# Performance work log

Measured on AMD Instinct MI355X. Metric: run time of the kernel, lower is better.

The kernel has to match this reference:

```python
import jax, jax.numpy as jnp
import numpy as np

INPUT_SIZE = 1024
NUM_QUBITS = 12
EMBED_SIZE = 2 ** NUM_QUBITS  # 4096
BATCH = 4096


def setup_inputs() -> dict:
    key = jax.random.key(0)
    k_x, k_w, k_p = jax.random.split(key, 3)
    x = jax.random.normal(k_x, (BATCH, INPUT_SIZE), dtype=jnp.float32)
    quantum_weights = jax.random.normal(k_w, (INPUT_SIZE, EMBED_SIZE), dtype=jnp.float32)
    quantum_phases = jax.random.normal(k_p, (INPUT_SIZE, NUM_QUBITS), dtype=jnp.float32)
    return {"x": x, "quantum_weights": quantum_weights, "quantum_phases": quantum_phases}


def reference(x, quantum_weights, quantum_phases):
    # Original: out[b] = Re( sum_j exp(i * mean(phases[j]) * x[b,j]) * W[j,:] ).
    # W is real, so the real part is sum_j cos(mean(phases[j]) * x[b,j]) * W[j,:],
    # i.e. a cosine-modulated matmul.
    phase_mean = jnp.mean(quantum_phases, axis=1)          # [input_size]
    coef = jnp.cos(x * phase_mean[None, :])                # [batch, input_size]
    return coef @ quantum_weights                          # [batch, embed_size]
```

## Files before the change

### kernel.cpp

```cpp
#include <hip/hip_runtime.h>
#include <hip/hip_bf16.h>


#define K_DIM 1024
#define N_DIM 4096
#define B_DIM 4096
#define NQ 12

typedef __attribute__((ext_vector_type(8))) _Float16 f16x8;
typedef __attribute__((ext_vector_type(4))) float f32x4;


__global__ void pm_kernel(const float* __restrict__ phases, float* __restrict__ pm) {
    int j = blockIdx.x * 256 + threadIdx.x;
    if (j < K_DIM) {
        float s = 0.f;
#pragma unroll
        for (int q = 0; q < NQ; ++q) s += phases[j * NQ + q];
        pm[j] = s * (1.0f / NQ);
    }
}

__global__ void asplit_kernel(const float* __restrict__ x, const float* __restrict__ pm,
                              char* __restrict__ Ah) {
    int i = blockIdx.x * 256 + threadIdx.x;
    int row = i >> 7;
    int k0  = (i & 127) << 3;
    const float* xp = x + ((size_t)row << 10) + k0;
    float4 xa = *(const float4*)xp;
    float4 xb = *(const float4*)(xp + 4);
    float4 pa = *(const float4*)(pm + k0);
    float4 pb = *(const float4*)(pm + k0 + 4);
    f16x8 hv;
    hv[0] = (_Float16)__cosf(xa.x * pa.x); hv[1] = (_Float16)__cosf(xa.y * pa.y);
    hv[2] = (_Float16)__cosf(xa.z * pa.z); hv[3] = (_Float16)__cosf(xa.w * pa.w);
    hv[4] = (_Float16)__cosf(xb.x * pb.x); hv[5] = (_Float16)__cosf(xb.y * pb.y);
    hv[6] = (_Float16)__cosf(xb.z * pb.z); hv[7] = (_Float16)__cosf(xb.w * pb.w);
    int tr = row >> 8, kt = k0 >> 6, khalf = (k0 & 63) >> 5;
    int r = row & 255, kk = k0 & 31;
    size_t base = ((size_t)tr * 16 + (size_t)kt) * 32768 + (size_t)khalf * 16384;
    int addr = ((r << 6) + (kk << 1)) ^ ((r & 7) << 4);
    *(f16x8*)(Ah + base + addr) = hv;
}

__global__ void wsplit_kernel(const float* __restrict__ W, char* __restrict__ Bf) {
    __shared__ float t[64][65];
    int n0 = blockIdx.x * 64, k0 = blockIdx.y * 64;
    int tid = threadIdx.x;
#pragma unroll
    for (int p = 0; p < 16; ++p) {
        int lin = p * 256 + tid;
        int kk = lin >> 6, nn = lin & 63;
        t[kk][nn] = W[(size_t)(k0 + kk) * N_DIM + n0 + nn];
    }
    __syncthreads();
    int tr = n0 >> 8, kt = k0 >> 6;
    size_t tbase = ((size_t)tr * 16 + (size_t)kt) * 32768;
#pragma unroll
    for (int p2 = 0; p2 < 2; ++p2) {
        int w = p2 * 256 + tid;
        int nn = w >> 3, oct = w & 7;
        int r = (n0 & 255) + nn;
        int khalf = oct >> 2;
        int kk = (oct & 3) * 8;
        f16x8 hv;
#pragma unroll
        for (int j = 0; j < 8; ++j) hv[j] = (_Float16)t[oct * 8 + j][nn];
        int addr = ((r << 6) + (kk << 1)) ^ ((r & 7) << 4);
        *(f16x8*)(Bf + tbase + (size_t)khalf * 16384 + addr) = hv;
    }
}

#define GLL16(g, l)                                                           \
    __builtin_amdgcn_global_load_lds(                                         \
        (const __attribute__((address_space(1))) void*)(g),                   \
        (__attribute__((address_space(3))) void*)(l), 16, 0, 0)

__global__ __launch_bounds__(512, 2) void gemm_kernel(
        const char* __restrict__ Ah, const char* __restrict__ Bf,
        float* __restrict__ C) {
    __shared__ char lds[131072];
    const int tid  = threadIdx.x;
    const int lane = tid & 63;
    const int wid  = tid >> 6;
    const int wm = wid >> 2, wn = wid & 3;
    const int fr   = lane & 15;
    const int colb = (lane >> 4) << 4;

    int wg  = blockIdx.x;
    int swz = (wg & 7) * 32 + (wg >> 3);
    const int by = swz >> 4, bx = swz & 15;

    const char* pA = Ah + (size_t)by * 16 * 32768;
    const char* pB = Bf + (size_t)bx * 16 * 32768;

    int aOff[8], bOff[4];
#pragma unroll
    for (int m = 0; m < 8; ++m) {
        int r = wm * 128 + m * 16 + fr;
        aOff[m] = ((r << 6) + colb) ^ ((r & 7) << 4);
    }
#pragma unroll
    for (int n = 0; n < 4; ++n) {
        int r = wn * 64 + n * 16 + fr;
        bOff[n] = ((r << 6) + colb) ^ ((r & 7) << 4);
    }

    const int so = tid << 4;

#pragma unroll
    for (int c = 0; c < 4; ++c) {
        const char* s = ((c & 1) ? pB : pA) + (c >> 1) * 16384;
        char* d = lds + c * 16384;
        GLL16(s + so, d + so);
        GLL16(s + 8192 + so, d + 8192 + so);
    }
    asm volatile("s_waitcnt vmcnt(4)" ::: "memory");
    __builtin_amdgcn_s_barrier();

    f32x4 acc[8][4];
#pragma unroll
    for (int m = 0; m < 8; ++m)
#pragma unroll
        for (int n = 0; n < 4; ++n)
            acc[m][n] = (f32x4){0.f, 0.f, 0.f, 0.f};

    for (int t = 0; t < 16; ++t) {
        const int cur = t & 1;
        const char* bufc = lds + cur * 65536;
        char* bufn = lds + (cur ^ 1) * 65536;
        const char* srcA = pA + (size_t)((t + 1) & 15) * 32768;
        const char* srcB = pB + (size_t)((t + 1) & 15) * 32768;

#pragma unroll
        for (int kh = 0; kh < 2; ++kh) {
            f16x8 bF[4];
#pragma unroll
            for (int mh = 0; mh < 2; ++mh) {
                if (mh == 0) {
#pragma unroll
                    for (int n = 0; n < 4; ++n)
                        bF[n] = *(const f16x8*)(bufc + 16384 + kh * 32768 + bOff[n]);
                }
                f16x8 aH[4];
#pragma unroll
                for (int q = 0; q < 4; ++q)
                    aH[q] = *(const f16x8*)(bufc + kh * 32768 + aOff[mh * 4 + q]);

                {
                    const int c = kh * 2 + mh;
                    const char* s = ((c & 1) ? srcB : srcA) + (c >> 1) * 16384;
                    char* d = bufn + c * 16384;
                    GLL16(s + so, d + so);
                    GLL16(s + 8192 + so, d + 8192 + so);
                }

                if (mh == 1)
                    asm volatile("s_waitcnt vmcnt(4)" ::: "memory");

                __builtin_amdgcn_s_barrier();

                __builtin_amdgcn_s_setprio(1);
#pragma unroll
                for (int q = 0; q < 4; ++q)
#pragma unroll
                    for (int n = 0; n < 4; ++n)
                        acc[mh * 4 + q][n] = __builtin_amdgcn_mfma_f32_16x16x32_f16(
                            aH[q], bF[n], acc[mh * 4 + q][n], 0, 0, 0);
                __builtin_amdgcn_s_setprio(0);

                __builtin_amdgcn_s_barrier();
            }
        }
    }

    const int crow0 = by * 256 + wm * 128 + ((lane >> 4) << 2);
    const int ccol0 = bx * 256 + wn * 64 + fr;
#pragma unroll
    for (int m = 0; m < 8; ++m)
#pragma unroll
        for (int n = 0; n < 4; ++n) {
            size_t base = (size_t)(crow0 + m * 16) * N_DIM + (size_t)(ccol0 + n * 16);
#pragma unroll
            for (int j = 0; j < 4; ++j)
                C[base + (size_t)j * N_DIM] = acc[m][n][j];
        }
}

extern "C" void kernel_launch(void* const* d_in, const int* in_sizes, int n_in,
                              void* d_out, int out_size, void* d_ws, size_t ws_size,
                              hipStream_t stream) {
    const float* x      = (const float*)d_in[0];
    const float* W      = (const float*)d_in[1];
    const float* phases = (const float*)d_in[2];
    float* out = (float*)d_out;

    char* ws = (char*)d_ws;
    float* pm = (float*)ws;
    char* Ah = ws + 65536;
    char* Bf = Ah + (size_t)8 * 1024 * 1024;

    pm_kernel<<<4, 256, 0, stream>>>(phases, pm);
    asplit_kernel<<<(B_DIM * (K_DIM / 8)) / 256, 256, 0, stream>>>(x, pm, Ah);
    wsplit_kernel<<<dim3(N_DIM / 64, K_DIM / 64), 256, 0, stream>>>(W, Bf);
    gemm_kernel<<<256, 512, 0, stream>>>(Ah, Bf, out);
}
```

Before: 131.9 us.

## Switch GEMM to 256x128 tiles with B fragments read directly from global

The GEMM kernel now uses 256-thread blocks computing 256x128 output tiles across 512 workgroups, with only the A operand staged in a 64KB double-buffered LDS region. B fragments are loaded straight from global memory into registers each K-step instead of going through LDS. This halves LDS use per block and simplifies the barrier schedule, which should allow more blocks per CU. The cost is uncoalesced, L2-dependent global reads for B and coarser __syncthreads sync in place of the finer interleaved barriers.

```diff
diff --git a/kernel.cpp b/kernel.cpp
--- a/kernel.cpp
+++ b/kernel.cpp
@@ -76,110 +76,102 @@
         (const __attribute__((address_space(1))) void*)(g),                   \
         (__attribute__((address_space(3))) void*)(l), 16, 0, 0)
 
-__global__ __launch_bounds__(512, 2) void gemm_kernel(
+__global__ __launch_bounds__(256, 2) void gemm_kernel(
         const char* __restrict__ Ah, const char* __restrict__ Bf,
         float* __restrict__ C) {
-    __shared__ char lds[131072];
+    __shared__ char lds[65536];
     const int tid  = threadIdx.x;
     const int lane = tid & 63;
     const int wid  = tid >> 6;
-    const int wm = wid >> 2, wn = wid & 3;
     const int fr   = lane & 15;
     const int colb = (lane >> 4) << 4;
 
     int wg  = blockIdx.x;
-    int swz = (wg & 7) * 32 + (wg >> 3);
-    const int by = swz >> 4, bx = swz & 15;
+    int swz = (wg & 7) * 64 + (wg >> 3);
+    const int by = swz >> 5;
+    const int bx = swz & 31;
 
     const char* pA = Ah + (size_t)by * 16 * 32768;
-    const char* pB = Bf + (size_t)bx * 16 * 32768;
+    const char* pB = Bf + (size_t)(bx >> 1) * 16 * 32768;
+    const int rB = (bx & 1) * 128;
 
-    int aOff[8], bOff[4];
+    int aOff[2][4];
 #pragma unroll
-    for (int m = 0; m < 8; ++m) {
-        int r = wm * 128 + m * 16 + fr;
-        aOff[m] = ((r << 6) + colb) ^ ((r & 7) << 4);
-    }
+    for (int kh = 0; kh < 2; ++kh)
 #pragma unroll
-    for (int n = 0; n < 4; ++n) {
-        int r = wn * 64 + n * 16 + fr;
-        bOff[n] = ((r << 6) + colb) ^ ((r & 7) << 4);
-    }
+        for (int m = 0; m < 4; ++m) {
+            int r = wid * 64 + m * 16 + fr;
+            aOff[kh][m] = kh * 16384 + ((((r << 6) + colb)) ^ ((r & 7) << 4));
+        }
+    int bOff[2][8];
+#pragma unroll
+    for (int kh = 0; kh < 2; ++kh)
+#pragma unroll
+        for (int n = 0; n < 8; ++n) {
+            int r = rB + n * 16 + fr;
+            bOff[kh][n] = kh * 16384 + ((((r << 6) + colb)) ^ ((r & 7) << 4));
+        }
 
     const int so = tid << 4;
 
 #pragma unroll
-    for (int c = 0; c < 4; ++c) {
-        const char* s = ((c & 1) ? pB : pA) + (c >> 1) * 16384;
-        char* d = lds + c * 16384;
-        GLL16(s + so, d + so);
-        GLL16(s + 8192 + so, d + 8192 + so);
-    }
-    asm volatile("s_waitcnt vmcnt(4)" ::: "memory");
-    __builtin_amdgcn_s_barrier();
+    for (int p = 0; p < 8; ++p)
+        GLL16(pA + p * 4096 + so, lds + p * 4096 + so);
 
-    f32x4 acc[8][4];
+    f32x4 acc[4][8];
 #pragma unroll
-    for (int m = 0; m < 8; ++m)
+    for (int m = 0; m < 4; ++m)
 #pragma unroll
-        for (int n = 0; n < 4; ++n)
+        for (int n = 0; n < 8; ++n)
             acc[m][n] = (f32x4){0.f, 0.f, 0.f, 0.f};
 
+    int cur = 0;
     for (int t = 0; t < 16; ++t) {
-        const int cur = t & 1;
-        const char* bufc = lds + cur * 65536;
-        char* bufn = lds + (cur ^ 1) * 65536;
-        const char* srcA = pA + (size_t)((t + 1) & 15) * 32768;
-        const char* srcB = pB + (size_t)((t + 1) & 15) * 32768;
+        __syncthreads();
 
+        const char* bChunk = pB + (size_t)t * 32768;
+        f16x8 bF[2][8];
+#pragma unroll
+        for (int kh = 0; kh < 2; ++kh)
+#pragma unroll
+            for (int n = 0; n < 8; ++n)
+                bF[kh][n] = *(const f16x8*)(bChunk + bOff[kh][n]);
+
+        {
+            const char* sA = pA + (size_t)((t + 1) & 15) * 32768;
+            char* d = lds + (cur ^ 1) * 32768;
+#pragma unroll
+            for (int p = 0; p < 8; ++p)
+                GLL16(sA + p * 4096 + so, d + p * 4096 + so);
+        }
+
+        const char* bufA = lds + cur * 32768;
 #pragma unroll
         for (int kh = 0; kh < 2; ++kh) {
-            f16x8 bF[4];
+            f16x8 aH[4];
 #pragma unroll
-            for (int mh = 0; mh < 2; ++mh) {
-                if (mh == 0) {
+            for (int m = 0; m < 4; ++m)
+                aH[m] = *(const f16x8*)(bufA + aOff[kh][m]);
+            __builtin_amdgcn_s_setprio(1);
 #pragma unroll
-                    for (int n = 0; n < 4; ++n)
-                        bF[n] = *(const f16x8*)(bufc + 16384 + kh * 32768 + bOff[n]);
-                }
-                f16x8 aH[4];
+            for (int m = 0; m < 4; ++m)
 #pragma unroll
-                for (int q = 0; q < 4; ++q)
-                    aH[q] = *(const f16x8*)(bufc + kh * 32768 + aOff[mh * 4 + q]);
+                for (int n = 0; n < 8; ++n)
+                    acc[m][n] = __builtin_amdgcn_mfma_f32_16x16x32_f16(
+                        aH[m], bF[kh][n], acc[m][n], 0, 0, 0);
+            __builtin_amdgcn_s_setprio(0);
+        }
 
-                {
-                    const int c = kh * 2 + mh;
-                    const char* s = ((c & 1) ? srcB : srcA) + (c >> 1) * 16384;
-                    char* d = bufn + c * 16384;
-                    GLL16(s + so, d + so);
-                    GLL16(s + 8192 + so, d + 8192 + so);
-                }
-
-                if (mh == 1)
-                    asm volatile("s_waitcnt vmcnt(4)" ::: "memory");
-
-                __builtin_amdgcn_s_barrier();
-
-                __builtin_amdgcn_s_setprio(1);
-#pragma unroll
-                for (int q = 0; q < 4; ++q)
-#pragma unroll
-                    for (int n = 0; n < 4; ++n)
-                        acc[mh * 4 + q][n] = __builtin_amdgcn_mfma_f32_16x16x32_f16(
-                            aH[q], bF[n], acc[mh * 4 + q][n], 0, 0, 0);
-                __builtin_amdgcn_s_setprio(0);
-
-                __builtin_amdgcn_s_barrier();
-            }
-        }
+        __syncthreads();
+        cur ^= 1;
     }
 
-    const int crow0 = by * 256 + wm * 128 + ((lane >> 4) << 2);
-    const int ccol0 = bx * 256 + wn * 64 + fr;
+    const int crow0 = by * 256 + wid * 64 + ((lane >> 4) << 2);
+    const int ccol0 = bx * 128 + fr;
 #pragma unroll
-    for (int m = 0; m < 8; ++m)
+    for (int m = 0; m < 4; ++m)
 #pragma unroll
-        for (int n = 0; n < 4; ++n) {
+        for (int n = 0; n < 8; ++n) {
             size_t base = (size_t)(crow0 + m * 16) * N_DIM + (size_t)(ccol0 + n * 16);
 #pragma unroll
             for (int j = 0; j < 4; ++j)
@@ -203,5 +195,5 @@
     pm_kernel<<<4, 256, 0, stream>>>(phases, pm);
     asplit_kernel<<<(B_DIM * (K_DIM / 8)) / 256, 256, 0, stream>>>(x, pm, Ah);
     wsplit_kernel<<<dim3(N_DIM / 64, K_DIM / 64), 256, 0, stream>>>(W, Bf);
-    gemm_kernel<<<256, 512, 0, stream>>>(Ah, Bf, out);
+    gemm_kernel<<<512, 256, 0, stream>>>(Ah, Bf, out);
 }
```

After: 131.7 us. About the same (-0.2%).
